# Optimization experiments

Measured on AMD Instinct MI355X. Metric: run time of the kernel, lower is better.

The kernel has to match this reference:

```python
import jax, jax.numpy as jnp
import numpy as np

NEG_INF = -4294967295.0  # -2**32 + 1, matches original padding value

def prelu(x, alpha):
    return jnp.where(x >= 0, x, alpha * x)

def setup_inputs() -> dict:
    key = jax.random.key(0)
    ks = jax.random.split(key, 12)
    B, T, D = 2048, 200, 64
    H0, H1 = 80, 40
    q = jax.random.normal(ks[0], (B, D), dtype=jnp.float32)
    k = jax.random.normal(ks[1], (B, T, D), dtype=jnp.float32)
    v = jax.random.normal(ks[2], (B, T, D), dtype=jnp.float32)
    mask = jax.random.randint(ks[3], (B, T), 0, 2, dtype=jnp.int32)
    Fin = 4 * D  # concat of q, k, q-k, q*k
    W0 = jax.random.normal(ks[4], (Fin, H0), dtype=jnp.float32) / np.sqrt(Fin)
    b0 = jnp.zeros((H0,), dtype=jnp.float32)
    a0 = jax.random.uniform(ks[5], (H0,), dtype=jnp.float32) * 0.25  # PReLU per-feature alpha
    W1 = jax.random.normal(ks[6], (H0, H1), dtype=jnp.float32) / np.sqrt(H0)
    b1 = jnp.zeros((H1,), dtype=jnp.float32)
    a1 = jax.random.uniform(ks[7], (H1,), dtype=jnp.float32) * 0.25
    Wo = jax.random.normal(ks[8], (H1, 1), dtype=jnp.float32) / np.sqrt(H1)
    bo = jnp.zeros((1,), dtype=jnp.float32)
    return {"q": q, "k": k, "v": v, "W0": W0, "b0": b0, "a0": a0,
            "W1": W1, "b1": b1, "a1": a1, "Wo": Wo, "bo": bo, "mask": mask}

def reference(q, k, v, W0, b0, a0, W1, b1, a1, Wo, bo, mask):
    # q: [B,D] -> broadcast to [B,T,D] (tile+reshape in original)
    qe = jnp.broadcast_to(q[:, None, :], k.shape)
    info = jnp.concatenate([qe, k, qe - k, qe * k], axis=-1)  # [B,T,4D]
    h = prelu(jnp.einsum('btf,fh->bth', info, W0) + b0, a0)    # [B,T,H0]
    h = prelu(jnp.einsum('bth,hg->btg', h, W1) + b1, a1)       # [B,T,H1]
    logits = (jnp.einsum('btg,go->bto', h, Wo) + bo)[..., 0]   # [B,T]
    logits = jnp.where(mask == 0, NEG_INF, logits)
    w = jax.nn.softmax(logits, axis=-1)                        # [B,T]
    out = jnp.einsum('bt,btd->bd', w, v)                       # [B,D]
    return out
```

## Files before the change

kernel.cpp:

```cpp
#include <hip/hip_runtime.h>
#include <math.h>

constexpr int D  = 64;
constexpr int T  = 200;
constexpr int H0 = 80;
constexpr int H1 = 40;
constexpr int BLOCK = 256;
constexpr float NEG_INF_V = -4294967295.0f;

typedef float f8 __attribute__((ext_vector_type(8)));
typedef short short8 __attribute__((ext_vector_type(8)));
typedef float f32x4 __attribute__((ext_vector_type(4)));

__device__ inline void split_bf16(float x, unsigned short& hi, unsigned short& lo) {
    union { float f; unsigned u; } a; a.f = x;
    unsigned r = a.u + 0x7FFF + ((a.u >> 16) & 1);
    hi = (unsigned short)(r >> 16);
    union { unsigned u; float f; } h; h.u = (unsigned)hi << 16;
    union { float f; unsigned u; } bvu; bvu.f = x - h.f;
    unsigned r2 = bvu.u + 0x7FFF + ((bvu.u >> 16) & 1);
    lo = (unsigned short)(r2 >> 16);
}

__global__ __launch_bounds__(256) void fold_frag(
    const float* __restrict__ q, const float* __restrict__ W0,
    const float* __restrict__ b0, const float* __restrict__ W1,
    short* __restrict__ wfHi, short* __restrict__ wfLo,
    float* __restrict__ biasq, short* __restrict__ w1fHi,
    short* __restrict__ w1fLo)
{
    const int b = blockIdx.x, tid = threadIdx.x;
    const float* qb = q + (size_t)b * D;

    for (int g = tid; g < 640; g += 256) {
        const int ks   = g / 320;
        const int r    = g - ks * 320;
        const int nt   = r >> 6;
        const int lane = r & 63;
        const int l16  = lane & 15, quad = lane >> 4;
        const int n    = nt * 16 + l16;
        short8 hi8, lo8;
        #pragma unroll
        for (int j = 0; j < 8; ++j) {
            const int kk = ks * 32 + quad * 8 + j;
            const float w = W0[(64 + kk) * H0 + n] - W0[(128 + kk) * H0 + n]
                          + qb[kk] * W0[(192 + kk) * H0 + n];
            unsigned short h, l; split_bf16(w, h, l);
            hi8[j] = (short)h; lo8[j] = (short)l;
        }
        const size_t o = ((size_t)(b * 2 + ks) * 5 + nt) * 512 + lane * 8;
        *(short8*)(wfHi + o) = hi8;
        *(short8*)(wfLo + o) = lo8;
    }
    if (tid < H0) {
        float acc = b0[tid];
        #pragma unroll 4
        for (int d = 0; d < D; ++d)
            acc = fmaf(qb[d], W0[d * H0 + tid] + W0[(128 + d) * H0 + tid], acc);
        biasq[(size_t)b * H0 + tid] = acc;
    }
    if (b == 0) {
        for (int g = tid; g < 576; g += 256) {
            const int k2s  = g / 192;
            const int r    = g - k2s * 192;
            const int nt2  = r >> 6;
            const int lane = r & 63;
            const int l16  = lane & 15, quad = lane >> 4;
            const int n    = nt2 * 16 + l16;
            short8 hi8, lo8;
            #pragma unroll
            for (int j = 0; j < 8; ++j) {
                const int k2 = k2s * 32 + quad * 8 + j;
                const float w = (k2 < H0 && n < H1) ? W1[k2 * H1 + n] : 0.0f;
                unsigned short h, l; split_bf16(w, h, l);
                hi8[j] = (short)h; lo8[j] = (short)l;
            }
            const size_t o = (size_t)(k2s * 3 + nt2) * 512 + lane * 8;
            *(short8*)(w1fHi + o) = hi8;
            *(short8*)(w1fLo + o) = lo8;
        }
    }
}

__global__ __launch_bounds__(BLOCK, 4) void attn_mfma(
    const float* __restrict__ k, const float* __restrict__ v,
    const short* __restrict__ wfHi, const short* __restrict__ wfLo,
    const float* __restrict__ biasq,
    const short* __restrict__ w1fHi, const short* __restrict__ w1fLo,
    const float* __restrict__ a0, const float* __restrict__ b1,
    const float* __restrict__ a1, const float* __restrict__ Wo,
    const float* __restrict__ bo, const int* __restrict__ mask,
    float* __restrict__ out)
{
    __shared__ unsigned short s_h0hi[4][16 * 96];
    __shared__ unsigned short s_h0lo[4][16 * 96];
    __shared__ float s_logits[208];
    __shared__ float s_biasq[H0];
    __shared__ float s_a0[H0];
    __shared__ float s_b1p[48], s_a1p[48], s_Wop[48];
    __shared__ float s_w[BLOCK];
    __shared__ float s_red[8];
    __shared__ float s_part[4][D];

    const int tid  = threadIdx.x;
    const int b    = blockIdx.x;
    const int wv   = tid >> 6;
    const int lane = tid & 63;
    const int l16  = lane & 15;
    const int quad = lane >> 4;

    if (tid < H0) { s_biasq[tid] = biasq[(size_t)b * H0 + tid]; s_a0[tid] = a0[tid]; }
    if (tid < 48) {
        s_b1p[tid] = (tid < H1) ? b1[tid] : 0.0f;
        s_a1p[tid] = (tid < H1) ? a1[tid] : 0.0f;
        s_Wop[tid] = (tid < H1) ? Wo[tid] : 0.0f;
    }
    __syncthreads();

    for (int mt = wv; mt < 13; mt += 4) {
        {
            const int r = lane >> 2, c = 80 + (lane & 3) * 4;
            *(unsigned long long*)&s_h0hi[wv][r * 96 + c] = 0ULL;
            *(unsigned long long*)&s_h0lo[wv][r * 96 + c] = 0ULL;
        }
        int row = mt * 16 + l16; if (row > T - 1) row = T - 1;
        const float* krow = k + ((size_t)b * T + row) * D + quad * 8;
        short8 a1hi[2], a1lo[2];
        #pragma unroll
        for (int ks = 0; ks < 2; ++ks) {
            float4 x0 = *(const float4*)(krow + ks * 32);
            float4 x1 = *(const float4*)(krow + ks * 32 + 4);
            float xs[8] = {x0.x, x0.y, x0.z, x0.w, x1.x, x1.y, x1.z, x1.w};
            #pragma unroll
            for (int j = 0; j < 8; ++j) {
                unsigned short h, l; split_bf16(xs[j], h, l);
                a1hi[ks][j] = (short)h; a1lo[ks][j] = (short)l;
            }
        }
        #pragma unroll 1
        for (int nt = 0; nt < 5; ++nt) {
            f32x4 acc = {0.0f, 0.0f, 0.0f, 0.0f};
            #pragma unroll
            for (int ks = 0; ks < 2; ++ks) {
                const size_t o = ((size_t)(b * 2 + ks) * 5 + nt) * 512 + lane * 8;
                short8 bh = *(const short8*)(wfHi + o);
                short8 bl = *(const short8*)(wfLo + o);
                acc = __builtin_amdgcn_mfma_f32_16x16x32_bf16(a1hi[ks], bh, acc, 0, 0, 0);
                acc = __builtin_amdgcn_mfma_f32_16x16x32_bf16(a1hi[ks], bl, acc, 0, 0, 0);
                acc = __builtin_amdgcn_mfma_f32_16x16x32_bf16(a1lo[ks], bh, acc, 0, 0, 0);
            }
            const int h = nt * 16 + l16;
            const float bq = s_biasq[h], al = s_a0[h];
            #pragma unroll
            for (int reg = 0; reg < 4; ++reg) {
                const float x  = acc[reg] + bq;
                const float h0 = (x >= 0.0f) ? x : al * x;
                unsigned short hh, hl; split_bf16(h0, hh, hl);
                const int addr = (quad * 4 + reg) * 96 + h;
                s_h0hi[wv][addr] = hh;
                s_h0lo[wv][addr] = hl;
            }
        }
        __asm__ __volatile__("s_waitcnt lgkmcnt(0)" ::: "memory");

        short8 a2hi[3], a2lo[3];
        #pragma unroll
        for (int k2s = 0; k2s < 3; ++k2s) {
            const int addr = l16 * 96 + k2s * 32 + quad * 8;
            a2hi[k2s] = *(const short8*)&s_h0hi[wv][addr];
            a2lo[k2s] = *(const short8*)&s_h0lo[wv][addr];
        }
        float part[4] = {0.0f, 0.0f, 0.0f, 0.0f};
        #pragma unroll 1
        for (int nt2 = 0; nt2 < 3; ++nt2) {
            f32x4 acc = {0.0f, 0.0f, 0.0f, 0.0f};
            #pragma unroll
            for (int k2s = 0; k2s < 3; ++k2s) {
                const size_t o = (size_t)(k2s * 3 + nt2) * 512 + lane * 8;
                short8 bh = *(const short8*)(w1fHi + o);
                short8 bl = *(const short8*)(w1fLo + o);
                acc = __builtin_amdgcn_mfma_f32_16x16x32_bf16(a2hi[k2s], bh, acc, 0, 0, 0);
                acc = __builtin_amdgcn_mfma_f32_16x16x32_bf16(a2hi[k2s], bl, acc, 0, 0, 0);
                acc = __builtin_amdgcn_mfma_f32_16x16x32_bf16(a2lo[k2s], bh, acc, 0, 0, 0);
            }
            const int g = nt2 * 16 + l16;
            const float bg = s_b1p[g], ag = s_a1p[g], wg = s_Wop[g];
            #pragma unroll
            for (int reg = 0; reg < 4; ++reg) {
                const float x  = acc[reg] + bg;
                const float hv = (x >= 0.0f) ? x : ag * x;
                part[reg] = fmaf(hv, wg, part[reg]);
            }
        }
        #pragma unroll
        for (int off = 1; off < 16; off <<= 1) {
            #pragma unroll
            for (int reg = 0; reg < 4; ++reg)
                part[reg] += __shfl_xor(part[reg], off);
        }
        if (l16 == 0) {
            float4 p = {part[0], part[1], part[2], part[3]};
            *(float4*)&s_logits[mt * 16 + quad * 4] = p;
        }
    }
    __asm__ __volatile__("s_waitcnt lgkmcnt(0)" ::: "memory");
    __syncthreads();

    float logit = -INFINITY;
    if (tid < T)
        logit = (mask[(size_t)b * T + tid] == 0) ? NEG_INF_V : s_logits[tid];

    float m = logit;
    #pragma unroll
    for (int off = 32; off > 0; off >>= 1) m = fmaxf(m, __shfl_xor(m, off));
    if (lane == 0) s_red[wv] = m;
    __syncthreads();
    m = fmaxf(fmaxf(s_red[0], s_red[1]), fmaxf(s_red[2], s_red[3]));
    const float e = expf(logit - m);
    s_w[tid] = e;
    float ssum = e;
    #pragma unroll
    for (int off = 32; off > 0; off >>= 1) ssum += __shfl_xor(ssum, off);
    if (lane == 0) s_red[4 + wv] = ssum;
    __syncthreads();
    const float inv = 1.0f / (s_red[4] + s_red[5] + s_red[6] + s_red[7]);

    const int d = tid & (D - 1);
    const int c = tid >> 6;
    constexpr int TC = T / 4;
    float acc2 = 0.0f;
    const float* vp = v + ((size_t)b * T + c * TC) * D + d;
    #pragma unroll 4
    for (int t = 0; t < TC; ++t)
        acc2 = fmaf(s_w[c * TC + t], vp[t * D], acc2);
    s_part[c][d] = acc2;
    __syncthreads();
    if (tid < D) {
        out[(size_t)b * D + tid] =
            (s_part[0][tid] + s_part[1][tid] + s_part[2][tid] + s_part[3][tid]) * inv;
    }
}

__global__ __launch_bounds__(256) void fold_small(
    const float* __restrict__ q, const float* __restrict__ W0,
    const float* __restrict__ b0, const float* __restrict__ W1,
    float* __restrict__ wbc, float* __restrict__ biasq, float* __restrict__ W1T)
{
    const int b = blockIdx.x, tid = threadIdx.x;
    const float* qb = q + (size_t)b * D;
    if (b == 0) {
        for (int i = tid; i < D * H0; i += 256)
            wbc[i] = W0[64 * H0 + i] - W0[128 * H0 + i];
        for (int i = tid; i < H0 * H1; i += 256) {
            int j = i / H1, g = i - j * H1;
            W1T[g * H0 + j] = W1[i];
        }
    }
    if (tid < H0) {
        float acc = b0[tid];
        #pragma unroll 4
        for (int d = 0; d < D; ++d)
            acc = fmaf(qb[d], W0[d * H0 + tid] + W0[(128 + d) * H0 + tid], acc);
        biasq[(size_t)b * H0 + tid] = acc;
    }
}

__global__ __launch_bounds__(BLOCK, 4) void attn_valu(
    const float* __restrict__ k, const float* __restrict__ v,
    const float* __restrict__ q, const float* __restrict__ wbc,
    const float* __restrict__ wB, const float* __restrict__ biasq,
    const float* __restrict__ W1T, const float* __restrict__ a0,
    const float* __restrict__ b1, const float* __restrict__ a1,
    const float* __restrict__ Wo, const float* __restrict__ bo,
    const int* __restrict__ mask, float* __restrict__ out)
{
    __shared__ float s_w[BLOCK];
    __shared__ float s_red[8];
    __shared__ float s_part[4][D];
    const int tid = threadIdx.x, b = blockIdx.x;
    const float* bq = biasq + (size_t)b * H0;
    const float* qb = q + (size_t)b * D;
    const int mval = (tid < T) ? mask[(size_t)b * T + tid] : 0;
    float logit;
    if (tid < T) {
        float acc[H0];
        #pragma unroll
        for (int h8 = 0; h8 < 10; ++h8) {
            f8 bv = *(const f8*)(bq + h8 * 8);
            #pragma unroll
            for (int j = 0; j < 8; ++j) acc[h8 * 8 + j] = bv[j];
        }
        const float4* kp4 = (const float4*)(k + ((size_t)b * T + tid) * D);
        #pragma unroll 1
        for (int d4 = 0; d4 < 16; ++d4) {
            const float4 kd = kp4[d4];
            const float* wr = wbc + (size_t)(d4 * 4) * H0;
            float4 qv = *(const float4*)(qb + d4 * 4);
            #pragma unroll
            for (int dd = 0; dd < 4; ++dd) {
                const float kv = (dd == 0) ? kd.x : (dd == 1) ? kd.y
                               : (dd == 2) ? kd.z : kd.w;
                const float qd = (dd == 0) ? qv.x : (dd == 1) ? qv.y
                               : (dd == 2) ? qv.z : qv.w;
                const float pd = kv * qd;
                const float* wdr = wB + (size_t)(d4 * 4 + dd) * H0;
                #pragma unroll
                for (int h8 = 0; h8 < 10; ++h8) {
                    f8 w = *(const f8*)(wr + dd * H0 + h8 * 8);
                    f8 w2 = *(const f8*)(wdr + h8 * 8);
                    #pragma unroll
                    for (int j = 0; j < 8; ++j) {
                        acc[h8 * 8 + j] = fmaf(kv, w[j], acc[h8 * 8 + j]);
                        acc[h8 * 8 + j] = fmaf(pd, w2[j], acc[h8 * 8 + j]);
                    }
                }
            }
        }
        #pragma unroll
        for (int h8 = 0; h8 < 10; ++h8) {
            f8 al = *(const f8*)(a0 + h8 * 8);
            #pragma unroll
            for (int j = 0; j < 8; ++j) {
                const float x = acc[h8 * 8 + j];
                acc[h8 * 8 + j] = (x >= 0.0f) ? x : al[j] * x;
            }
        }
        float lg = bo[0];
        #pragma unroll 1
        for (int g = 0; g < H1; ++g) {
            const float* wg = W1T + g * H0;
            float sum = b1[g];
            #pragma unroll
            for (int h8 = 0; h8 < 10; ++h8) {
                f8 w = *(const f8*)(wg + h8 * 8);
                #pragma unroll
                for (int j = 0; j < 8; ++j) sum = fmaf(acc[h8 * 8 + j], w[j], sum);
            }
            const float hv = (sum >= 0.0f) ? sum : a1[g] * sum;
            lg = fmaf(hv, Wo[g], lg);
        }
        logit = (mval == 0) ? NEG_INF_V : lg;
    } else logit = -INFINITY;
    float m = logit;
    #pragma unroll
    for (int off = 32; off > 0; off >>= 1) m = fmaxf(m, __shfl_xor(m, off));
    if ((tid & 63) == 0) s_red[tid >> 6] = m;
    __syncthreads();
    m = fmaxf(fmaxf(s_red[0], s_red[1]), fmaxf(s_red[2], s_red[3]));
    const float e = expf(logit - m);
    s_w[tid] = e;
    float ssum = e;
    #pragma unroll
    for (int off = 32; off > 0; off >>= 1) ssum += __shfl_xor(ssum, off);
    if ((tid & 63) == 0) s_red[4 + (tid >> 6)] = ssum;
    __syncthreads();
    const float inv = 1.0f / (s_red[4] + s_red[5] + s_red[6] + s_red[7]);
    const int d = tid & (D - 1);
    const int c = tid >> 6;
    constexpr int TC = T / 4;
    float acc2 = 0.0f;
    const float* vp = v + ((size_t)b * T + c * TC) * D + d;
    #pragma unroll 4
    for (int t = 0; t < TC; ++t) acc2 = fmaf(s_w[c * TC + t], vp[t * D], acc2);
    s_part[c][d] = acc2;
    __syncthreads();
    if (tid < D)
        out[(size_t)b * D + tid] =
            (s_part[0][tid] + s_part[1][tid] + s_part[2][tid] + s_part[3][tid]) * inv;
}

extern "C" void kernel_launch(void* const* d_in, const int* in_sizes, int n_in,
                              void* d_out, int out_size, void* d_ws, size_t ws_size,
                              hipStream_t stream) {
    const float* q  = (const float*)d_in[0];
    const float* k  = (const float*)d_in[1];
    const float* v  = (const float*)d_in[2];
    const float* W0 = (const float*)d_in[3];
    const float* b0 = (const float*)d_in[4];
    const float* a0 = (const float*)d_in[5];
    const float* W1 = (const float*)d_in[6];
    const float* b1 = (const float*)d_in[7];
    const float* a1 = (const float*)d_in[8];
    const float* Wo = (const float*)d_in[9];
    const float* bo = (const float*)d_in[10];
    const int*  mask = (const int*)d_in[11];
    float* out = (float*)d_out;

    const int B = in_sizes[0] / D;

    const size_t n_wf   = (size_t)B * 5120;
    const size_t need = n_wf * 2 * 2 + (size_t)B * H0 * 4 + 4608 * 2 * 2;
    if (ws_size >= need) {
        short* wfHi  = (short*)d_ws;
        short* wfLo  = wfHi + n_wf;
        float* biasq = (float*)(wfLo + n_wf);
        short* w1fHi = (short*)(biasq + (size_t)B * H0);
        short* w1fLo = w1fHi + 4608;
        fold_frag<<<dim3(B), dim3(256), 0, stream>>>(
            q, W0, b0, W1, wfHi, wfLo, biasq, w1fHi, w1fLo);
        attn_mfma<<<dim3(B), dim3(BLOCK), 0, stream>>>(
            k, v, wfHi, wfLo, biasq, w1fHi, w1fLo,
            a0, b1, a1, Wo, bo, mask, out);
    } else {
        float* wbc   = (float*)d_ws;
        float* biasq = wbc + (size_t)D * H0;
        float* W1T   = biasq + (size_t)B * H0;
        const float* w0d = W0 + 192 * H0;
        fold_small<<<dim3(B), dim3(256), 0, stream>>>(q, W0, b0, W1, wbc, biasq, W1T);
        attn_valu<<<dim3(B), dim3(BLOCK), 0, stream>>>(
            k, v, q, wbc, w0d, biasq, W1T, a0, b1, a1, Wo, bo, mask, out);
    }
}
```

Before: 324.1 us.

## Fuse weight-folding into attention kernel, stage fragments in LDS, prefetch k rows

```diff
diff --git a/kernel.cpp b/kernel.cpp
--- a/kernel.cpp
+++ b/kernel.cpp
@@ -8,7 +8,6 @@
 constexpr int BLOCK = 256;
 constexpr float NEG_INF_V = -4294967295.0f;
 
-typedef float f8 __attribute__((ext_vector_type(8)));
 typedef short short8 __attribute__((ext_vector_type(8)));
 typedef float f32x4 __attribute__((ext_vector_type(4)));
 
@@ -22,78 +21,20 @@
     lo = (unsigned short)(r2 >> 16);
 }
 
-__global__ __launch_bounds__(256) void fold_frag(
-    const float* __restrict__ q, const float* __restrict__ W0,
-    const float* __restrict__ b0, const float* __restrict__ W1,
-    short* __restrict__ wfHi, short* __restrict__ wfLo,
-    float* __restrict__ biasq, short* __restrict__ w1fHi,
-    short* __restrict__ w1fLo)
+__global__ __launch_bounds__(BLOCK, 2) void attn_fused(
+    const float* __restrict__ q, const float* __restrict__ k,
+    const float* __restrict__ v, const float* __restrict__ W0,
+    const float* __restrict__ b0, const float* __restrict__ a0,
+    const float* __restrict__ W1, const float* __restrict__ b1,
+    const float* __restrict__ a1, const float* __restrict__ Wo,
+    const int* __restrict__ mask, float* __restrict__ out)
 {
-    const int b = blockIdx.x, tid = threadIdx.x;
-    const float* qb = q + (size_t)b * D;
-
-    for (int g = tid; g < 640; g += 256) {
-        const int ks   = g / 320;
-        const int r    = g - ks * 320;
-        const int nt   = r >> 6;
-        const int lane = r & 63;
-        const int l16  = lane & 15, quad = lane >> 4;
-        const int n    = nt * 16 + l16;
-        short8 hi8, lo8;
-        #pragma unroll
-        for (int j = 0; j < 8; ++j) {
-            const int kk = ks * 32 + quad * 8 + j;
-            const float w = W0[(64 + kk) * H0 + n] - W0[(128 + kk) * H0 + n]
-                          + qb[kk] * W0[(192 + kk) * H0 + n];
-            unsigned short h, l; split_bf16(w, h, l);
-            hi8[j] = (short)h; lo8[j] = (short)l;
-        }
-        const size_t o = ((size_t)(b * 2 + ks) * 5 + nt) * 512 + lane * 8;
-        *(short8*)(wfHi + o) = hi8;
-        *(short8*)(wfLo + o) = lo8;
-    }
-    if (tid < H0) {
-        float acc = b0[tid];
-        #pragma unroll 4
-        for (int d = 0; d < D; ++d)
-            acc = fmaf(qb[d], W0[d * H0 + tid] + W0[(128 + d) * H0 + tid], acc);
-        biasq[(size_t)b * H0 + tid] = acc;
-    }
-    if (b == 0) {
-        for (int g = tid; g < 576; g += 256) {
-            const int k2s  = g / 192;
-            const int r    = g - k2s * 192;
-            const int nt2  = r >> 6;
-            const int lane = r & 63;
-            const int l16  = lane & 15, quad = lane >> 4;
-            const int n    = nt2 * 16 + l16;
-            short8 hi8, lo8;
-            #pragma unroll
-            for (int j = 0; j < 8; ++j) {
-                const int k2 = k2s * 32 + quad * 8 + j;
-                const float w = (k2 < H0 && n < H1) ? W1[k2 * H1 + n] : 0.0f;
-                unsigned short h, l; split_bf16(w, h, l);
-                hi8[j] = (short)h; lo8[j] = (short)l;
-            }
-            const size_t o = (size_t)(k2s * 3 + nt2) * 512 + lane * 8;
-            *(short8*)(w1fHi + o) = hi8;
-            *(short8*)(w1fLo + o) = lo8;
-        }
-    }
-}
-
-__global__ __launch_bounds__(BLOCK, 4) void attn_mfma(
-    const float* __restrict__ k, const float* __restrict__ v,
-    const short* __restrict__ wfHi, const short* __restrict__ wfLo,
-    const float* __restrict__ biasq,
-    const short* __restrict__ w1fHi, const short* __restrict__ w1fLo,
-    const float* __restrict__ a0, const float* __restrict__ b1,
-    const float* __restrict__ a1, const float* __restrict__ Wo,
-    const float* __restrict__ bo, const int* __restrict__ mask,
-    float* __restrict__ out)
-{
-    __shared__ unsigned short s_h0hi[4][16 * 96];
-    __shared__ unsigned short s_h0lo[4][16 * 96];
+    __shared__ unsigned short s_wfHi[5120];
+    __shared__ unsigned short s_wfLo[5120];
+    __shared__ unsigned short s_w1Hi[4608];
+    __shared__ unsigned short s_w1Lo[4608];
+    __shared__ unsigned short s_h0hi[4][16 * 80];
+    __shared__ unsigned short s_h0lo[4][16 * 80];
     __shared__ float s_logits[208];
     __shared__ float s_biasq[H0];
     __shared__ float s_a0[H0];
@@ -108,8 +49,50 @@
     const int lane = tid & 63;
     const int l16  = lane & 15;
     const int quad = lane >> 4;
-
-    if (tid < H0) { s_biasq[tid] = biasq[(size_t)b * H0 + tid]; s_a0[tid] = a0[tid]; }
+    const float* qb = q + (size_t)b * D;
+
+    const int mval = (tid < T) ? mask[(size_t)b * T + tid] : 0;
+    float4 kc[4];
+    {
+        int row = wv * 16 + l16; if (row > T - 1) row = T - 1;
+        const float* kr = k + ((size_t)b * T + row) * D + quad * 8;
+        kc[0] = *(const float4*)(kr);
+        kc[1] = *(const float4*)(kr + 4);
+        kc[2] = *(const float4*)(kr + 32);
+        kc[3] = *(const float4*)(kr + 36);
+    }
+
+    const float* Wk = W0 + 64 * H0;
+    const float* Wd = W0 + 128 * H0;
+    const float* Wp = W0 + 192 * H0;
+    #pragma unroll 4
+    for (int it = 0; it < 20; ++it) {
+        const int e  = it * 256 + tid;
+        const int kk = e / 80, n = e - kk * 80;
+        const float w = Wk[e] - Wd[e] + qb[kk] * Wp[e];
+        unsigned short h, l; split_bf16(w, h, l);
+        const int off = (((kk >> 5) * 5 + (n >> 4)) << 9)
+                      + ((((kk >> 3) & 3) * 16 + (n & 15)) << 3) + (kk & 7);
+        s_wfHi[off] = h; s_wfLo[off] = l;
+    }
+    #pragma unroll 4
+    for (int it = 0; it < 18; ++it) {
+        const int e  = it * 256 + tid;
+        const int k2 = e / 48, n = e - k2 * 48;
+        const float w = (k2 < H0 && n < H1) ? W1[k2 * H1 + n] : 0.0f;
+        unsigned short h, l; split_bf16(w, h, l);
+        const int off = (((k2 >> 5) * 3 + (n >> 4)) << 9)
+                      + ((((k2 >> 3) & 3) * 16 + (n & 15)) << 3) + (k2 & 7);
+        s_w1Hi[off] = h; s_w1Lo[off] = l;
+    }
+    if (tid < H0) {
+        float acc = b0[tid];
+        #pragma unroll 8
+        for (int d = 0; d < D; ++d)
+            acc = fmaf(qb[d], W0[d * H0 + tid] + W0[(128 + d) * H0 + tid], acc);
+        s_biasq[tid] = acc;
+        s_a0[tid]    = a0[tid];
+    }
     if (tid < 48) {
         s_b1p[tid] = (tid < H1) ? b1[tid] : 0.0f;
         s_a1p[tid] = (tid < H1) ? a1[tid] : 0.0f;
@@ -118,33 +101,35 @@
     __syncthreads();
 
     for (int mt = wv; mt < 13; mt += 4) {
-        {
-            const int r = lane >> 2, c = 80 + (lane & 3) * 4;
-            *(unsigned long long*)&s_h0hi[wv][r * 96 + c] = 0ULL;
-            *(unsigned long long*)&s_h0lo[wv][r * 96 + c] = 0ULL;
-        }
-        int row = mt * 16 + l16; if (row > T - 1) row = T - 1;
-        const float* krow = k + ((size_t)b * T + row) * D + quad * 8;
+        float4 kn[4];
+        const bool hasNext = (mt + 4 < 13);
+        if (hasNext) {
+            int row = (mt + 4) * 16 + l16; if (row > T - 1) row = T - 1;
+            const float* kr = k + ((size_t)b * T + row) * D + quad * 8;
+            kn[0] = *(const float4*)(kr);
+            kn[1] = *(const float4*)(kr + 4);
+            kn[2] = *(const float4*)(kr + 32);
+            kn[3] = *(const float4*)(kr + 36);
+        }
         short8 a1hi[2], a1lo[2];
         #pragma unroll
         for (int ks = 0; ks < 2; ++ks) {
-            float4 x0 = *(const float4*)(krow + ks * 32);
-            float4 x1 = *(const float4*)(krow + ks * 32 + 4);
-            float xs[8] = {x0.x, x0.y, x0.z, x0.w, x1.x, x1.y, x1.z, x1.w};
+            float xs[8] = {kc[ks*2].x, kc[ks*2].y, kc[ks*2].z, kc[ks*2].w,
+                           kc[ks*2+1].x, kc[ks*2+1].y, kc[ks*2+1].z, kc[ks*2+1].w};
             #pragma unroll
             for (int j = 0; j < 8; ++j) {
                 unsigned short h, l; split_bf16(xs[j], h, l);
                 a1hi[ks][j] = (short)h; a1lo[ks][j] = (short)l;
             }
         }
-        #pragma unroll 1
+        #pragma unroll
         for (int nt = 0; nt < 5; ++nt) {
             f32x4 acc = {0.0f, 0.0f, 0.0f, 0.0f};
             #pragma unroll
             for (int ks = 0; ks < 2; ++ks) {
-                const size_t o = ((size_t)(b * 2 + ks) * 5 + nt) * 512 + lane * 8;
-                short8 bh = *(const short8*)(wfHi + o);
-                short8 bl = *(const short8*)(wfLo + o);
+                const int off = (ks * 5 + nt) * 512 + lane * 8;
+                short8 bh = *(const short8*)&s_wfHi[off];
+                short8 bl = *(const short8*)&s_wfLo[off];
                 acc = __builtin_amdgcn_mfma_f32_16x16x32_bf16(a1hi[ks], bh, acc, 0, 0, 0);
                 acc = __builtin_amdgcn_mfma_f32_16x16x32_bf16(a1hi[ks], bl, acc, 0, 0, 0);
                 acc = __builtin_amdgcn_mfma_f32_16x16x32_bf16(a1lo[ks], bh, acc, 0, 0, 0);
@@ -153,10 +138,10 @@
             const float bq = s_biasq[h], al = s_a0[h];
             #pragma unroll
             for (int reg = 0; reg < 4; ++reg) {
-                const float x  = acc[reg] + bq;
-                const float h0 = (x >= 0.0f) ? x : al * x;
-                unsigned short hh, hl; split_bf16(h0, hh, hl);
-                const int addr = (quad * 4 + reg) * 96 + h;
+                const float x   = acc[reg] + bq;
+                const float h0v = (x >= 0.0f) ? x : al * x;
+                unsigned short hh, hl; split_bf16(h0v, hh, hl);
+                const int addr = (quad * 4 + reg) * 80 + h;
                 s_h0hi[wv][addr] = hh;
                 s_h0lo[wv][addr] = hl;
             }
@@ -166,19 +151,24 @@
         short8 a2hi[3], a2lo[3];
         #pragma unroll
         for (int k2s = 0; k2s < 3; ++k2s) {
-            const int addr = l16 * 96 + k2s * 32 + quad * 8;
-            a2hi[k2s] = *(const short8*)&s_h0hi[wv][addr];
-            a2lo[k2s] = *(const short8*)&s_h0lo[wv][addr];
+            if (k2s < 2 || quad < 2) {
+                const int addr = l16 * 80 + k2s * 32 + quad * 8;
+                a2hi[k2s] = *(const short8*)&s_h0hi[wv][addr];
+                a2lo[k2s] = *(const short8*)&s_h0lo[wv][addr];
+            } else {
+                short8 z = {0, 0, 0, 0, 0, 0, 0, 0};
+                a2hi[k2s] = z; a2lo[k2s] = z;
+            }
         }
         float part[4] = {0.0f, 0.0f, 0.0f, 0.0f};
-        #pragma unroll 1
+        #pragma unroll
         for (int nt2 = 0; nt2 < 3; ++nt2) {
             f32x4 acc = {0.0f, 0.0f, 0.0f, 0.0f};
             #pragma unroll
             for (int k2s = 0; k2s < 3; ++k2s) {
-                const size_t o = (size_t)(k2s * 3 + nt2) * 512 + lane * 8;
-                short8 bh = *(const short8*)(w1fHi + o);
-                short8 bl = *(const short8*)(w1fLo + o);
+                const int off = (k2s * 3 + nt2) * 512 + lane * 8;
+                short8 bh = *(const short8*)&s_w1Hi[off];
+                short8 bl = *(const short8*)&s_w1Lo[off];
                 acc = __builtin_amdgcn_mfma_f32_16x16x32_bf16(a2hi[k2s], bh, acc, 0, 0, 0);
                 acc = __builtin_amdgcn_mfma_f32_16x16x32_bf16(a2hi[k2s], bl, acc, 0, 0, 0);
                 acc = __builtin_amdgcn_mfma_f32_16x16x32_bf16(a2lo[k2s], bh, acc, 0, 0, 0);
@@ -202,13 +192,17 @@
             float4 p = {part[0], part[1], part[2], part[3]};
             *(float4*)&s_logits[mt * 16 + quad * 4] = p;
         }
+        if (hasNext) {
+            #pragma unroll
+            for (int i = 0; i < 4; ++i) kc[i] = kn[i];
+        }
     }
     __asm__ __volatile__("s_waitcnt lgkmcnt(0)" ::: "memory");
     __syncthreads();
 
     float logit = -INFINITY;
     if (tid < T)
-        logit = (mask[(size_t)b * T + tid] == 0) ? NEG_INF_V : s_logits[tid];
+        logit = (mval == 0) ? NEG_INF_V : s_logits[tid];
 
     float m = logit;
     #pragma unroll
@@ -230,7 +224,7 @@
     constexpr int TC = T / 4;
     float acc2 = 0.0f;
     const float* vp = v + ((size_t)b * T + c * TC) * D + d;
-    #pragma unroll 4
+    #pragma unroll 10
     for (int t = 0; t < TC; ++t)
         acc2 = fmaf(s_w[c * TC + t], vp[t * D], acc2);
     s_part[c][d] = acc2;
@@ -239,134 +233,6 @@
         out[(size_t)b * D + tid] =
             (s_part[0][tid] + s_part[1][tid] + s_part[2][tid] + s_part[3][tid]) * inv;
     }
-}
-
-__global__ __launch_bounds__(256) void fold_small(
-    const float* __restrict__ q, const float* __restrict__ W0,
-    const float* __restrict__ b0, const float* __restrict__ W1,
-    float* __restrict__ wbc, float* __restrict__ biasq, float* __restrict__ W1T)
-{
-    const int b = blockIdx.x, tid = threadIdx.x;
-    const float* qb = q + (size_t)b * D;
-    if (b == 0) {
-        for (int i = tid; i < D * H0; i += 256)
-            wbc[i] = W0[64 * H0 + i] - W0[128 * H0 + i];
-        for (int i = tid; i < H0 * H1; i += 256) {
-            int j = i / H1, g = i - j * H1;
-            W1T[g * H0 + j] = W1[i];
-        }
-    }
-    if (tid < H0) {
-        float acc = b0[tid];
-        #pragma unroll 4
-        for (int d = 0; d < D; ++d)
-            acc = fmaf(qb[d], W0[d * H0 + tid] + W0[(128 + d) * H0 + tid], acc);
-        biasq[(size_t)b * H0 + tid] = acc;
-    }
-}
-
-__global__ __launch_bounds__(BLOCK, 4) void attn_valu(
-    const float* __restrict__ k, const float* __restrict__ v,
-    const float* __restrict__ q, const float* __restrict__ wbc,
-    const float* __restrict__ wB, const float* __restrict__ biasq,
-    const float* __restrict__ W1T, const float* __restrict__ a0,
-    const float* __restrict__ b1, const float* __restrict__ a1,
-    const float* __restrict__ Wo, const float* __restrict__ bo,
-    const int* __restrict__ mask, float* __restrict__ out)
-{
-    __shared__ float s_w[BLOCK];
-    __shared__ float s_red[8];
-    __shared__ float s_part[4][D];
-    const int tid = threadIdx.x, b = blockIdx.x;
-    const float* bq = biasq + (size_t)b * H0;
-    const float* qb = q + (size_t)b * D;
-    const int mval = (tid < T) ? mask[(size_t)b * T + tid] : 0;
-    float logit;
-    if (tid < T) {
-        float acc[H0];
-        #pragma unroll
-        for (int h8 = 0; h8 < 10; ++h8) {
-            f8 bv = *(const f8*)(bq + h8 * 8);
-            #pragma unroll
-            for (int j = 0; j < 8; ++j) acc[h8 * 8 + j] = bv[j];
-        }
-        const float4* kp4 = (const float4*)(k + ((size_t)b * T + tid) * D);
-        #pragma unroll 1
-        for (int d4 = 0; d4 < 16; ++d4) {
-            const float4 kd = kp4[d4];
-            const float* wr = wbc + (size_t)(d4 * 4) * H0;
-            float4 qv = *(const float4*)(qb + d4 * 4);
-            #pragma unroll
-            for (int dd = 0; dd < 4; ++dd) {
-                const float kv = (dd == 0) ? kd.x : (dd == 1) ? kd.y
-                               : (dd == 2) ? kd.z : kd.w;
-                const float qd = (dd == 0) ? qv.x : (dd == 1) ? qv.y
-                               : (dd == 2) ? qv.z : qv.w;
-                const float pd = kv * qd;
-                const float* wdr = wB + (size_t)(d4 * 4 + dd) * H0;
-                #pragma unroll
-                for (int h8 = 0; h8 < 10; ++h8) {
-                    f8 w = *(const f8*)(wr + dd * H0 + h8 * 8);
-                    f8 w2 = *(const f8*)(wdr + h8 * 8);
-                    #pragma unroll
-                    for (int j = 0; j < 8; ++j) {
-                        acc[h8 * 8 + j] = fmaf(kv, w[j], acc[h8 * 8 + j]);
-                        acc[h8 * 8 + j] = fmaf(pd, w2[j], acc[h8 * 8 + j]);
-                    }
-                }
-            }
-        }
-        #pragma unroll
-        for (int h8 = 0; h8 < 10; ++h8) {
-            f8 al = *(const f8*)(a0 + h8 * 8);
-            #pragma unroll
-            for (int j = 0; j < 8; ++j) {
-                const float x = acc[h8 * 8 + j];
-                acc[h8 * 8 + j] = (x >= 0.0f) ? x : al[j] * x;
-            }
-        }
-        float lg = bo[0];
-        #pragma unroll 1
-        for (int g = 0; g < H1; ++g) {
-            const float* wg = W1T + g * H0;
-            float sum = b1[g];
-            #pragma unroll
-            for (int h8 = 0; h8 < 10; ++h8) {
-                f8 w = *(const f8*)(wg + h8 * 8);
-                #pragma unroll
-                for (int j = 0; j < 8; ++j) sum = fmaf(acc[h8 * 8 + j], w[j], sum);
-            }
-            const float hv = (sum >= 0.0f) ? sum : a1[g] * sum;
-            lg = fmaf(hv, Wo[g], lg);
-        }
-        logit = (mval == 0) ? NEG_INF_V : lg;
-    } else logit = -INFINITY;
-    float m = logit;
-    #pragma unroll
-    for (int off = 32; off > 0; off >>= 1) m = fmaxf(m, __shfl_xor(m, off));
-    if ((tid & 63) == 0) s_red[tid >> 6] = m;
-    __syncthreads();
-    m = fmaxf(fmaxf(s_red[0], s_red[1]), fmaxf(s_red[2], s_red[3]));
-    const float e = expf(logit - m);
-    s_w[tid] = e;
-    float ssum = e;
-    #pragma unroll
-    for (int off = 32; off > 0; off >>= 1) ssum += __shfl_xor(ssum, off);
-    if ((tid & 63) == 0) s_red[4 + (tid >> 6)] = ssum;
-    __syncthreads();
-    const float inv = 1.0f / (s_red[4] + s_red[5] + s_red[6] + s_red[7]);
-    const int d = tid & (D - 1);
-    const int c = tid >> 6;
-    constexpr int TC = T / 4;
-    float acc2 = 0.0f;
-    const float* vp = v + ((size_t)b * T + c * TC) * D + d;
-    #pragma unroll 4
-    for (int t = 0; t < TC; ++t) acc2 = fmaf(s_w[c * TC + t], vp[t * D], acc2);
-    s_part[c][d] = acc2;
-    __syncthreads();
-    if (tid < D)
-        out[(size_t)b * D + tid] =
-            (s_part[0][tid] + s_part[1][tid] + s_part[2][tid] + s_part[3][tid]) * inv;
 }
 
 extern "C" void kernel_launch(void* const* d_in, const int* in_sizes, int n_in,
@@ -382,32 +248,11 @@
     const float* b1 = (const float*)d_in[7];
     const float* a1 = (const float*)d_in[8];
     const float* Wo = (const float*)d_in[9];
-    const float* bo = (const float*)d_in[10];
     const int*  mask = (const int*)d_in[11];
     float* out = (float*)d_out;
 
     const int B = in_sizes[0] / D;
 
-    const size_t n_wf   = (size_t)B * 5120;
-    const size_t need = n_wf * 2 * 2 + (size_t)B * H0 * 4 + 4608 * 2 * 2;
-    if (ws_size >= need) {
-        short* wfHi  = (short*)d_ws;
-        short* wfLo  = wfHi + n_wf;
-        float* biasq = (float*)(wfLo + n_wf);
-        short* w1fHi = (short*)(biasq + (size_t)B * H0);
-        short* w1fLo = w1fHi + 4608;
-        fold_frag<<<dim3(B), dim3(256), 0, stream>>>(
-            q, W0, b0, W1, wfHi, wfLo, biasq, w1fHi, w1fLo);
-        attn_mfma<<<dim3(B), dim3(BLOCK), 0, stream>>>(
-            k, v, wfHi, wfLo, biasq, w1fHi, w1fLo,
-            a0, b1, a1, Wo, bo, mask, out);
-    } else {
-        float* wbc   = (float*)d_ws;
-        float* biasq = wbc + (size_t)D * H0;
-        float* W1T   = biasq + (size_t)B * H0;
-        const float* w0d = W0 + 192 * H0;
-        fold_small<<<dim3(B), dim3(256), 0, stream>>>(q, W0, b0, W1, wbc, biasq, W1T);
-        attn_valu<<<dim3(B), dim3(BLOCK), 0, stream>>>(
-            k, v, q, wbc, w0d, biasq, W1T, a0, b1, a1, Wo, bo, mask, out);
-    }
+    attn_fused<<<dim3(B), dim3(BLOCK), 0, stream>>>(
+        q, k, v, W0, b0, a0, W1, b1, a1, Wo, mask, out);
 }
```

New measurement: 296.7 us. -8.4%, faster.
